# Performance work log

Measured on AMD Instinct MI355X. Metric: run time of the kernel, lower is better.

## Reference

```python
import jax, jax.numpy as jnp
import numpy as np

EPS = 1e-10
COMMITMENT_COST = 0.25


def setup_inputs() -> dict:
    key = jax.random.key(0)
    k1, k2 = jax.random.split(key)
    inputs = jax.random.normal(k1, (64, 64, 32, 32), dtype=jnp.float32)
    # nn.init.uniform_(weight, -1.0, 1.0)
    embeddings = jax.random.uniform(k2, (1024, 64), dtype=jnp.float32, minval=-1.0, maxval=1.0)
    return {"inputs": inputs, "embeddings": embeddings}


def reference(inputs, embeddings):
    B, C, H, W = inputs.shape  # C == embedding_dim
    K = embeddings.shape[0]
    x = jnp.transpose(inputs, (0, 2, 3, 1)).reshape(-1, C)  # [N, D]
    d = (jnp.sum(x * x, axis=1, keepdims=True)
         - 2.0 * (x @ embeddings.T)
         + jnp.sum(embeddings * embeddings, axis=1))  # [N, K]
    idx = jnp.argmin(d, axis=1)  # [N]
    # one-hot @ embeddings == gather
    q = jnp.take(embeddings, idx, axis=0)  # [N, D]
    x4 = x.reshape(B, H, W, C)
    q4 = q.reshape(B, H, W, C)
    e_latent = jnp.mean((jax.lax.stop_gradient(q4) - x4) ** 2)
    q_latent = jnp.mean((q4 - jax.lax.stop_gradient(x4)) ** 2)
    loss = q_latent + COMMITMENT_COST * e_latent
    # straight-through estimator
    st = x4 + jax.lax.stop_gradient(q4 - x4)
    # avg_probs = mean of one-hot encodings == normalized histogram
    n = idx.shape[0]
    avg_probs = jnp.zeros((K,), dtype=jnp.float32).at[idx].add(1.0) / n
    perplexity = jnp.exp(-jnp.sum(avg_probs * jnp.log(avg_probs + EPS)))
    quantized = jnp.transpose(st, (0, 3, 1, 2))
    return quantized, loss, perplexity
```

## Files before the change

### kernel.cpp

```cpp
#include <hip/hip_runtime.h>

#define N_TOTAL   65536
#define HW_SZ     1024
#define CDIM      64
#define K_CODES   1024
#define OUT_ELEMS 4194304
#define QT        256
#define NCHUNK    4
#define TAU       0.004f


typedef __attribute__((ext_vector_type(8))) short short8;
typedef __attribute__((ext_vector_type(4))) float f32x4;

__device__ __forceinline__ unsigned short f2bf(float x) {
    unsigned u = __float_as_uint(x);
    return (unsigned short)((u + 0x7FFFu + ((u >> 16) & 1u)) >> 16);
}
__device__ __forceinline__ float bf2f(unsigned short h) {
    return __uint_as_float(((unsigned)h) << 16);
}
__device__ __forceinline__ void gload_lds16(const void* g, void* l) {
    __builtin_amdgcn_global_load_lds(
        (const __attribute__((address_space(1))) void*)g,
        (__attribute__((address_space(3))) void*)l, 16, 0, 0);
}

__global__ void k_prep(const float* __restrict__ emb, float* __restrict__ enorm,
                       short* __restrict__ btab, unsigned int* __restrict__ hist) {
    int gid = blockIdx.x * 256 + threadIdx.x;
    int r  = gid >> 4;
    int d0 = (gid & 15) * 4;
    float4 v = *(const float4*)(emb + gid * 4);
    float s = v.x * v.x + v.y * v.y + v.z * v.z + v.w * v.w;
#pragma unroll
    for (int off = 1; off < 16; off <<= 1) s += __shfl_xor(s, off, 64);
    if ((gid & 15) == 0) enorm[r] = s;

    float vv[4] = {v.x, v.y, v.z, v.w};
    short h[4], l[4];
#pragma unroll
    for (int j = 0; j < 4; ++j) {
        unsigned short hh = f2bf(vv[j]);
        h[j] = (short)hh;
        l[j] = (short)f2bf(vv[j] - bf2f(hh));
    }
    int base = (r >> 4) * 2048 + (d0 >> 5) * 1024
             + ((((d0 >> 3) & 3) * 16 + (r & 15)) * 8) + (d0 & 7);
    *(short4*)&btab[base]       = make_short4(h[0], h[1], h[2], h[3]);
    *(short4*)&btab[base + 512] = make_short4(l[0], l[1], l[2], l[3]);

    if (gid < K_CODES) hist[gid] = 0u;
}

__global__ __launch_bounds__(256, 1)
void k_argmin(const float* __restrict__ x, const float* __restrict__ emb,
              const short* __restrict__ btab, const float* __restrict__ enorm,
              unsigned int* __restrict__ hist, float* __restrict__ partials,
              float* __restrict__ out) {
    __shared__ __align__(16) short bufs[2][16 * 2048];
    __shared__ __align__(16) float ens[K_CODES];
    __shared__ float xnorm[QT];
    __shared__ float rd1[QT];
    __shared__ float rd2[QT];
    __shared__ int   ri[QT];
    __shared__ int   flist[QT];
    __shared__ __align__(16) float xqf[CDIM];
    __shared__ float wdd[4];
    __shared__ int   wii[4];
    __shared__ float spw[4];
    __shared__ int   nflag;
    float* tile = (float*)bufs;

    const int tid  = threadIdx.x;
    const int lane = tid & 63;
    const int w    = tid >> 6;
    const int quad = lane >> 4;
    const int col  = lane & 15;

    const int n0  = blockIdx.x * QT;
    const int b   = n0 >> 10;
    const int hw0 = n0 & 1023;

    auto stage_async = [&](int c, int bsel) {
        const short* src = btab + c * (16 * 2048);
#pragma unroll
        for (int i = 0; i < 16; ++i) {
            int idx = i * 256 + tid;
            gload_lds16(&src[idx * 8], (void*)&bufs[bsel][idx * 8]);
        }
    };

    stage_async(0, 0);
    gload_lds16(&enorm[tid * 4], (void*)&ens[tid * 4]);

    const float* xb = x + b * (CDIM * HW_SZ) + hw0 + col;
    short8 afr[4][2][2];
#pragma unroll
    for (int rt = 0; rt < 4; ++rt) {
        float nloc = 0.f;
#pragma unroll
        for (int kc = 0; kc < 2; ++kc) {
#pragma unroll
            for (int j = 0; j < 8; ++j) {
                int c0 = (kc * 4 + quad) * 8 + j;
                float v = xb[c0 * HW_SZ + w * 64 + rt * 16];
                unsigned short hh = f2bf(v);
                afr[rt][kc][0][j] = (short)hh;
                afr[rt][kc][1][j] = (short)f2bf(v - bf2f(hh));
                nloc = __builtin_fmaf(v, v, nloc);
            }
        }
        nloc += __shfl_xor(nloc, 16, 64);
        nloc += __shfl_xor(nloc, 32, 64);
        if (quad == 0) xnorm[w * 64 + rt * 16 + col] = nloc;
    }

    float d1[16], d2[16];
    int   i1[16];
#pragma unroll
    for (int t = 0; t < 16; ++t) { d1[t] = 3.4e38f; d2[t] = 3.4e38f; i1[t] = 0; }

    __syncthreads();

    for (int c = 0; c < NCHUNK; ++c) {
        if (c + 1 < NCHUNK) stage_async(c + 1, (c + 1) & 1);
        const short* bs = &bufs[c & 1][0];
        const int cbase = c * 256;
#pragma unroll 4
        for (int ctl = 0; ctl < 16; ++ctl) {
            const short* fp = bs + ctl * 2048 + lane * 8;
            short8 B00 = *(const short8*)(fp);
            short8 B01 = *(const short8*)(fp + 512);
            short8 B10 = *(const short8*)(fp + 1024);
            short8 B11 = *(const short8*)(fp + 1536);
            const int   mycode = cbase + ctl * 16 + col;
            const float en     = ens[mycode];
#pragma unroll
            for (int rt = 0; rt < 4; ++rt) {
                f32x4 acc = {0.f, 0.f, 0.f, 0.f};
                acc = __builtin_amdgcn_mfma_f32_16x16x32_bf16(afr[rt][0][1], B00, acc, 0, 0, 0);
                acc = __builtin_amdgcn_mfma_f32_16x16x32_bf16(afr[rt][0][0], B01, acc, 0, 0, 0);
                acc = __builtin_amdgcn_mfma_f32_16x16x32_bf16(afr[rt][0][0], B00, acc, 0, 0, 0);
                acc = __builtin_amdgcn_mfma_f32_16x16x32_bf16(afr[rt][1][1], B10, acc, 0, 0, 0);
                acc = __builtin_amdgcn_mfma_f32_16x16x32_bf16(afr[rt][1][0], B11, acc, 0, 0, 0);
                acc = __builtin_amdgcn_mfma_f32_16x16x32_bf16(afr[rt][1][0], B10, acc, 0, 0, 0);
#pragma unroll
                for (int reg = 0; reg < 4; ++reg) {
                    int t = rt * 4 + reg;
                    float d   = __builtin_fmaf(acc[reg], -2.f, en);
                    float d1o = d1[t];
                    d2[t] = __builtin_amdgcn_fmed3f(d, d1o, d2[t]);
                    d1[t] = fminf(d, d1o);
                    i1[t] = (d < d1o) ? mycode : i1[t];
                }
            }
        }
        __syncthreads();
    }

#pragma unroll
    for (int t = 0; t < 16; ++t) {
        float a1 = d1[t], a2 = d2[t];
        int ai = i1[t];
#pragma unroll
        for (int off = 1; off < 16; off <<= 1) {
            float o1 = __shfl_xor(a1, off, 64);
            float o2 = __shfl_xor(a2, off, 64);
            int   oi = __shfl_xor(ai, off, 64);
            if (o1 < a1 || (o1 == a1 && oi < ai)) {
                float loser = a1; a2 = fminf(fminf(a2, o2), loser); a1 = o1; ai = oi;
            } else {
                a2 = fminf(fminf(a2, o2), o1);
            }
        }
        d1[t] = a1; d2[t] = a2; i1[t] = ai;
    }

    if (tid == 0) nflag = 0;
    if (col == 0) {
#pragma unroll
        for (int rt = 0; rt < 4; ++rt)
#pragma unroll
            for (int reg = 0; reg < 4; ++reg) {
                int t = rt * 4 + reg;
                int m = w * 64 + rt * 16 + quad * 4 + reg;
                rd1[m] = d1[t];
                rd2[m] = d2[t];
                ri [m] = i1[t];
            }
    }
    __syncthreads();

    if (tid < QT) {
        if (rd2[tid] - rd1[tid] < TAU) {
            int slot = atomicAdd(&nflag, 1);
            flist[slot] = tid;
        }
    }
    __syncthreads();

    for (int f = 0; f < nflag; ++f) {
        const int q = flist[f];
        if (tid < CDIM) xqf[tid] = x[b * (CDIM * HW_SZ) + tid * HW_SZ + hw0 + q];
        __syncthreads();
        float dm = 3.4e38f; int im = 0;
#pragma unroll
        for (int cd = 0; cd < 4; ++cd) {
            const int k = tid + cd * 256;
            const float4* er = (const float4*)(emb + k * CDIM);
            const float4* xr = (const float4*)xqf;
            float dot = 0.f;
#pragma unroll
            for (int c4 = 0; c4 < 16; ++c4) {
                float4 e = er[c4], xv = xr[c4];
                dot += e.x * xv.x + e.y * xv.y + e.z * xv.z + e.w * xv.w;
            }
            float d = ens[k] - 2.f * dot;
            if (d < dm) { dm = d; im = k; }
        }
#pragma unroll
        for (int off = 1; off < 64; off <<= 1) {
            float od = __shfl_xor(dm, off, 64);
            int   oi = __shfl_xor(im, off, 64);
            if (od < dm || (od == dm && oi < im)) { dm = od; im = oi; }
        }
        if (lane == 0) { wdd[w] = dm; wii[w] = im; }
        __syncthreads();
        if (tid == 0) {
            float bd = wdd[0]; int bi = wii[0];
#pragma unroll
            for (int ww = 1; ww < 4; ++ww)
                if (wdd[ww] < bd || (wdd[ww] == bd && wii[ww] < bi)) { bd = wdd[ww]; bi = wii[ww]; }
            rd1[q] = bd; ri[q] = bi;
        }
        __syncthreads();
    }

    {
        int ai = ri[tid];
        atomicAdd(&hist[ai], 1u);
        float sp = rd1[tid] + xnorm[tid];
#pragma unroll
        for (int off = 32; off; off >>= 1) sp += __shfl_down(sp, off, 64);
        if (lane == 0) spw[w] = sp;
    }
    __syncthreads();
    if (tid == 0) partials[blockIdx.x] = spw[0] + spw[1] + spw[2] + spw[3];

#pragma unroll
    for (int h = 0; h < 4; ++h) {
        {
            int q = tid >> 2, j = tid & 3;
            int code = ri[h * 64 + q];
            int ct = code >> 4, cl = code & 15;
            int kc = j >> 1;
            int qa = (2 * j) & 3, qb = (2 * j + 1) & 3;
            const short* tb = btab + ct * 2048 + kc * 1024;
            short8 hi0 = *(const short8*)&tb[(qa * 16 + cl) * 8];
            short8 hi1 = *(const short8*)&tb[(qb * 16 + cl) * 8];
            short8 lo0 = *(const short8*)&tb[512 + (qa * 16 + cl) * 8];
            short8 lo1 = *(const short8*)&tb[512 + (qb * 16 + cl) * 8];
            float* dst = &tile[q * 72 + j * 16];
#pragma unroll
            for (int k = 0; k < 8; ++k) {
                dst[k]     = bf2f((unsigned short)hi0[k]) + bf2f((unsigned short)lo0[k]);
                dst[8 + k] = bf2f((unsigned short)hi1[k]) + bf2f((unsigned short)lo1[k]);
            }
        }
        __syncthreads();
        {
            int c = tid >> 2;
            float* ob = out + b * (CDIM * HW_SZ) + c * HW_SZ + hw0 + h * 64;
#pragma unroll
            for (int p = 0; p < 4; ++p) {
                int q = ((tid & 3) + p * 4) * 4;
                float4 v;
                v.x = tile[(q + 0) * 72 + c];
                v.y = tile[(q + 1) * 72 + c];
                v.z = tile[(q + 2) * 72 + c];
                v.w = tile[(q + 3) * 72 + c];
                *(float4*)&ob[q] = v;
            }
        }
        if (h < 3) __syncthreads();
    }
}

__global__ void k_final(const float* __restrict__ partials,
                        const unsigned int* __restrict__ hist,
                        float* __restrict__ out) {
    int tid = threadIdx.x;
    float ss = partials[tid];
    float s = 0.f;
#pragma unroll
    for (int i = 0; i < 4; ++i) {
        float p = (float)hist[i * 256 + tid] * (1.0f / 65536.0f);
        s += p * logf(p + 1e-10f);
    }
    __shared__ float fin[8];
#pragma unroll
    for (int off = 32; off; off >>= 1) {
        ss += __shfl_down(ss, off, 64);
        s  += __shfl_down(s, off, 64);
    }
    if ((tid & 63) == 0) { fin[tid >> 6] = ss; fin[4 + (tid >> 6)] = s; }
    __syncthreads();
    if (tid == 0) {
        float sse = fin[0] + fin[1] + fin[2] + fin[3];
        float ent = fin[4] + fin[5] + fin[6] + fin[7];
        out[OUT_ELEMS]     = 1.25f * sse * (1.0f / (float)OUT_ELEMS);
        out[OUT_ELEMS + 1] = expf(-ent);
    }
}

extern "C" void kernel_launch(void* const* d_in, const int* in_sizes, int n_in,
                              void* d_out, int out_size, void* d_ws, size_t ws_size,
                              hipStream_t stream) {
    const float* x   = (const float*)d_in[0];
    const float* emb = (const float*)d_in[1];
    float* out = (float*)d_out;
    char* ws = (char*)d_ws;
    float*        enorm    = (float*)(ws);
    unsigned int* hist     = (unsigned int*)(ws + 4096);
    float*        partials = (float*)(ws + 8192);
    short*        btab     = (short*)(ws + 12288);

    k_prep  <<<64, 256, 0, stream>>>(emb, enorm, btab, hist);
    k_argmin<<<N_TOTAL / QT, 256, 0, stream>>>(x, emb, btab, enorm, hist, partials, out);
    k_final <<<1, 256, 0, stream>>>(partials, hist, out);
}
```

Before: 132.3 us.

## Use 512-thread blocks with 8 waves each covering 32 query rows

Doubles the threads per block in the argmin kernel, so each of 8 waves handles 32 query rows instead of 64. Per-thread register state (A fragments, running top-2 distances) is halved. The codebook staging, the exact fallback search and the output transpose are redistributed across 512 threads. The six-MFMA chain per row tile is also split into two independent accumulators, shortening dependency latency. More waves per CU should hide LDS and MFMA latency better, at the cost of each wave re-reading the same B fragments from LDS for fewer rows.

```diff
diff --git a/kernel.cpp b/kernel.cpp
--- a/kernel.cpp
+++ b/kernel.cpp
@@ -53,7 +53,7 @@
     if (gid < K_CODES) hist[gid] = 0u;
 }
 
-__global__ __launch_bounds__(256, 1)
+__global__ __launch_bounds__(512, 2)
 void k_argmin(const float* __restrict__ x, const float* __restrict__ emb,
               const short* __restrict__ btab, const float* __restrict__ enorm,
               unsigned int* __restrict__ hist, float* __restrict__ partials,
@@ -66,8 +66,8 @@
     __shared__ int   ri[QT];
     __shared__ int   flist[QT];
     __shared__ __align__(16) float xqf[CDIM];
-    __shared__ float wdd[4];
-    __shared__ int   wii[4];
+    __shared__ float wdd[8];
+    __shared__ int   wii[8];
     __shared__ float spw[4];
     __shared__ int   nflag;
     float* tile = (float*)bufs;
@@ -85,26 +85,26 @@
     auto stage_async = [&](int c, int bsel) {
         const short* src = btab + c * (16 * 2048);
 #pragma unroll
-        for (int i = 0; i < 16; ++i) {
-            int idx = i * 256 + tid;
+        for (int i = 0; i < 8; ++i) {
+            int idx = i * 512 + tid;
             gload_lds16(&src[idx * 8], (void*)&bufs[bsel][idx * 8]);
         }
     };
 
     stage_async(0, 0);
-    gload_lds16(&enorm[tid * 4], (void*)&ens[tid * 4]);
+    if (tid < 256) gload_lds16(&enorm[tid * 4], (void*)&ens[tid * 4]);
 
     const float* xb = x + b * (CDIM * HW_SZ) + hw0 + col;
-    short8 afr[4][2][2];
-#pragma unroll
-    for (int rt = 0; rt < 4; ++rt) {
+    short8 afr[2][2][2];
+#pragma unroll
+    for (int rt = 0; rt < 2; ++rt) {
         float nloc = 0.f;
 #pragma unroll
         for (int kc = 0; kc < 2; ++kc) {
 #pragma unroll
             for (int j = 0; j < 8; ++j) {
                 int c0 = (kc * 4 + quad) * 8 + j;
-                float v = xb[c0 * HW_SZ + w * 64 + rt * 16];
+                float v = xb[c0 * HW_SZ + w * 32 + rt * 16];
                 unsigned short hh = f2bf(v);
                 afr[rt][kc][0][j] = (short)hh;
                 afr[rt][kc][1][j] = (short)f2bf(v - bf2f(hh));
@@ -113,13 +113,13 @@
         }
         nloc += __shfl_xor(nloc, 16, 64);
         nloc += __shfl_xor(nloc, 32, 64);
-        if (quad == 0) xnorm[w * 64 + rt * 16 + col] = nloc;
-    }
-
-    float d1[16], d2[16];
-    int   i1[16];
-#pragma unroll
-    for (int t = 0; t < 16; ++t) { d1[t] = 3.4e38f; d2[t] = 3.4e38f; i1[t] = 0; }
+        if (quad == 0) xnorm[w * 32 + rt * 16 + col] = nloc;
+    }
+
+    float d1[8], d2[8];
+    int   i1[8];
+#pragma unroll
+    for (int t = 0; t < 8; ++t) { d1[t] = 3.4e38f; d2[t] = 3.4e38f; i1[t] = 0; }
 
     __syncthreads();
 
@@ -137,18 +137,20 @@
             const int   mycode = cbase + ctl * 16 + col;
             const float en     = ens[mycode];
 #pragma unroll
-            for (int rt = 0; rt < 4; ++rt) {
-                f32x4 acc = {0.f, 0.f, 0.f, 0.f};
-                acc = __builtin_amdgcn_mfma_f32_16x16x32_bf16(afr[rt][0][1], B00, acc, 0, 0, 0);
-                acc = __builtin_amdgcn_mfma_f32_16x16x32_bf16(afr[rt][0][0], B01, acc, 0, 0, 0);
-                acc = __builtin_amdgcn_mfma_f32_16x16x32_bf16(afr[rt][0][0], B00, acc, 0, 0, 0);
-                acc = __builtin_amdgcn_mfma_f32_16x16x32_bf16(afr[rt][1][1], B10, acc, 0, 0, 0);
-                acc = __builtin_amdgcn_mfma_f32_16x16x32_bf16(afr[rt][1][0], B11, acc, 0, 0, 0);
-                acc = __builtin_amdgcn_mfma_f32_16x16x32_bf16(afr[rt][1][0], B10, acc, 0, 0, 0);
+            for (int rt = 0; rt < 2; ++rt) {
+                f32x4 a0 = {0.f, 0.f, 0.f, 0.f};
+                f32x4 a1 = {0.f, 0.f, 0.f, 0.f};
+                a0 = __builtin_amdgcn_mfma_f32_16x16x32_bf16(afr[rt][0][1], B00, a0, 0, 0, 0);
+                a1 = __builtin_amdgcn_mfma_f32_16x16x32_bf16(afr[rt][1][1], B10, a1, 0, 0, 0);
+                a0 = __builtin_amdgcn_mfma_f32_16x16x32_bf16(afr[rt][0][0], B01, a0, 0, 0, 0);
+                a1 = __builtin_amdgcn_mfma_f32_16x16x32_bf16(afr[rt][1][0], B11, a1, 0, 0, 0);
+                a0 = __builtin_amdgcn_mfma_f32_16x16x32_bf16(afr[rt][0][0], B00, a0, 0, 0, 0);
+                a1 = __builtin_amdgcn_mfma_f32_16x16x32_bf16(afr[rt][1][0], B10, a1, 0, 0, 0);
 #pragma unroll
                 for (int reg = 0; reg < 4; ++reg) {
                     int t = rt * 4 + reg;
-                    float d   = __builtin_fmaf(acc[reg], -2.f, en);
+                    float dot = a0[reg] + a1[reg];
+                    float d   = __builtin_fmaf(dot, -2.f, en);
                     float d1o = d1[t];
                     d2[t] = __builtin_amdgcn_fmed3f(d, d1o, d2[t]);
                     d1[t] = fminf(d, d1o);
@@ -160,7 +162,7 @@
     }
 
 #pragma unroll
-    for (int t = 0; t < 16; ++t) {
+    for (int t = 0; t < 8; ++t) {
         float a1 = d1[t], a2 = d2[t];
         int ai = i1[t];
 #pragma unroll
@@ -180,11 +182,11 @@
     if (tid == 0) nflag = 0;
     if (col == 0) {
 #pragma unroll
-        for (int rt = 0; rt < 4; ++rt)
+        for (int rt = 0; rt < 2; ++rt)
 #pragma unroll
             for (int reg = 0; reg < 4; ++reg) {
                 int t = rt * 4 + reg;
-                int m = w * 64 + rt * 16 + quad * 4 + reg;
+                int m = w * 32 + rt * 16 + quad * 4 + reg;
                 rd1[m] = d1[t];
                 rd2[m] = d2[t];
                 ri [m] = i1[t];
@@ -206,8 +208,8 @@
         __syncthreads();
         float dm = 3.4e38f; int im = 0;
 #pragma unroll
-        for (int cd = 0; cd < 4; ++cd) {
-            const int k = tid + cd * 256;
+        for (int cd = 0; cd < 2; ++cd) {
+            const int k = tid + cd * 512;
             const float4* er = (const float4*)(emb + k * CDIM);
             const float4* xr = (const float4*)xqf;
             float dot = 0.f;
@@ -230,14 +232,14 @@
         if (tid == 0) {
             float bd = wdd[0]; int bi = wii[0];
 #pragma unroll
-            for (int ww = 1; ww < 4; ++ww)
+            for (int ww = 1; ww < 8; ++ww)
                 if (wdd[ww] < bd || (wdd[ww] == bd && wii[ww] < bi)) { bd = wdd[ww]; bi = wii[ww]; }
             rd1[q] = bd; ri[q] = bi;
         }
         __syncthreads();
     }
 
-    {
+    if (tid < QT) {
         int ai = ri[tid];
         atomicAdd(&hist[ai], 1u);
         float sp = rd1[tid] + xnorm[tid];
@@ -251,30 +253,25 @@
 #pragma unroll
     for (int h = 0; h < 4; ++h) {
         {
-            int q = tid >> 2, j = tid & 3;
+            int q = tid >> 3, j8 = tid & 7;
             int code = ri[h * 64 + q];
             int ct = code >> 4, cl = code & 15;
-            int kc = j >> 1;
-            int qa = (2 * j) & 3, qb = (2 * j + 1) & 3;
+            int kc = j8 >> 2, qd = j8 & 3;
             const short* tb = btab + ct * 2048 + kc * 1024;
-            short8 hi0 = *(const short8*)&tb[(qa * 16 + cl) * 8];
-            short8 hi1 = *(const short8*)&tb[(qb * 16 + cl) * 8];
-            short8 lo0 = *(const short8*)&tb[512 + (qa * 16 + cl) * 8];
-            short8 lo1 = *(const short8*)&tb[512 + (qb * 16 + cl) * 8];
-            float* dst = &tile[q * 72 + j * 16];
-#pragma unroll
-            for (int k = 0; k < 8; ++k) {
-                dst[k]     = bf2f((unsigned short)hi0[k]) + bf2f((unsigned short)lo0[k]);
-                dst[8 + k] = bf2f((unsigned short)hi1[k]) + bf2f((unsigned short)lo1[k]);
-            }
+            short8 hi = *(const short8*)&tb[(qd * 16 + cl) * 8];
+            short8 lo = *(const short8*)&tb[512 + (qd * 16 + cl) * 8];
+            float* dst = &tile[q * 72 + j8 * 8];
+#pragma unroll
+            for (int k = 0; k < 8; ++k)
+                dst[k] = bf2f((unsigned short)hi[k]) + bf2f((unsigned short)lo[k]);
         }
         __syncthreads();
         {
-            int c = tid >> 2;
+            int c = tid >> 3;
             float* ob = out + b * (CDIM * HW_SZ) + c * HW_SZ + hw0 + h * 64;
 #pragma unroll
-            for (int p = 0; p < 4; ++p) {
-                int q = ((tid & 3) + p * 4) * 4;
+            for (int p = 0; p < 2; ++p) {
+                int q = ((tid & 7) + p * 8) * 4;
                 float4 v;
                 v.x = tile[(q + 0) * 72 + c];
                 v.y = tile[(q + 1) * 72 + c];
@@ -327,6 +324,6 @@
     short*        btab     = (short*)(ws + 12288);
 
     k_prep  <<<64, 256, 0, stream>>>(emb, enorm, btab, hist);
-    k_argmin<<<N_TOTAL / QT, 256, 0, stream>>>(x, emb, btab, enorm, hist, partials, out);
+    k_argmin<<<N_TOTAL / QT, 512, 0, stream>>>(x, emb, btab, enorm, hist, partials, out);
     k_final <<<1, 256, 0, stream>>>(partials, hist, out);
 }
```

Result: faster. 127.1 us (-4.0%).
